# Kernel optimization log

Hardware: AMD Instinct MI355X
Metric: run time of the kernel (lower is better)

## Reference

```python
import jax, jax.numpy as jnp
import numpy as np

D_MODEL, N_HEADS, HEAD_DIM, D_STATE, CHUNK, N_GROUPS = 3584, 112, 64, 64, 256, 2


def setup_inputs() -> dict:
    key = jax.random.key(0)
    ks = jax.random.split(key, 8)
    b, l = 1, 4096
    inner = N_HEADS * HEAD_DIM
    scale = 0.02  # keep activations well-scaled (nn.Linear-ish init)
    return {
        "hidden_states": jax.random.normal(ks[0], (b, l, D_MODEL), jnp.float32),
        "W_in": jax.random.normal(ks[1], (2 * inner, D_MODEL), jnp.float32) * scale,
        "W_out": jax.random.normal(ks[2], (D_MODEL, inner), jnp.float32) * scale,
        "A_log": jax.random.normal(ks[3], (N_HEADS,), jnp.float32),
        "D": jnp.ones((N_HEADS,), jnp.float32),
        "dt_bias": jax.random.normal(ks[4], (N_HEADS,), jnp.float32),
        "B": jax.random.normal(ks[5], (b, l, N_GROUPS, D_STATE), jnp.float32),
        "C": jax.random.normal(ks[6], (b, l, N_GROUPS, D_STATE), jnp.float32),
    }


def _segsum(x):
    # x: [..., T] -> [..., T, T]; segsum[i,j] = sum_{j<k<=i} x[k], -inf above diag
    T = x.shape[-1]
    cs = jnp.cumsum(x, axis=-1)
    diff = cs[..., :, None] - cs[..., None, :]
    mask = jnp.tril(jnp.ones((T, T), bool))
    return jnp.where(mask, diff, -jnp.inf)


def reference(hidden_states, W_in, W_out, A_log, D, dt_bias, B, C):
    b, l, _ = hidden_states.shape
    h, p, n, c = N_HEADS, HEAD_DIM, D_STATE, CHUNK
    nc = l // c

    xz = hidden_states @ W_in.T                       # [b,l,2*h*p]
    x, z = jnp.split(xz, 2, axis=-1)
    x = x.reshape(b, l, h, p)

    dt = jnp.full((b, l, h), 0.1, hidden_states.dtype)  # module uses constant 0.1
    A = -jnp.exp(A_log)                                  # [h]
    dt_sp = jax.nn.softplus(dt + dt_bias)                # [b,l,h]

    # expand group-shared B/C to per-head
    Bh = jnp.repeat(B, h // N_GROUPS, axis=2)            # [b,l,h,n]
    Ch = jnp.repeat(C, h // N_GROUPS, axis=2)

    xdt = x * dt_sp[..., None]                           # discretized input dt*x

    # chunked views: k = chunk index, i/j = position within chunk
    xc = xdt.reshape(b, nc, c, h, p)
    Bc = Bh.reshape(b, nc, c, h, n)
    Cc = Ch.reshape(b, nc, c, h, n)
    dA = (dt_sp * A).reshape(b, nc, c, h).transpose(0, 3, 1, 2)  # [b,h,nc,c]
    dA_cs = jnp.cumsum(dA, axis=-1)                               # [b,h,nc,c]

    # 1) intra-chunk (diagonal blocks)
    L = jnp.exp(_segsum(dA))                                      # [b,h,nc,c,c]
    Y_diag = jnp.einsum('bkihn,bkjhn,bhkij,bkjhp->bkihp', Cc, Bc, L, xc)

    # 2) per-chunk end states
    decay_states = jnp.exp(dA_cs[..., -1:] - dA_cs)               # [b,h,nc,c]
    states = jnp.einsum('bkjhn,bhkj,bkjhp->bkhpn', Bc, decay_states, xc)

    # 3) inter-chunk recurrence: S_k = exp(sum dA_k) * S_{k-1} + states_k
    chunk_decay = jnp.exp(dA_cs[..., -1])                         # [b,h,nc]

    def step(carry, inp):
        dec, st = inp                      # dec: [b,h], st: [b,h,p,n]
        new = carry * dec[..., None, None] + st
        return new, carry                  # emit state ENTERING this chunk

    _, prev = jax.lax.scan(
        step,
        jnp.zeros_like(states[:, 0]),
        (chunk_decay.transpose(2, 0, 1), states.transpose(1, 0, 2, 3, 4)),
    )
    prev = prev.transpose(1, 0, 2, 3, 4)                          # [b,nc,h,p,n]

    # 4) inter-chunk output contribution
    Y_off = jnp.einsum('bkihn,bkhpn,bhki->bkihp', Cc, prev, jnp.exp(dA_cs))

    y = (Y_diag + Y_off).reshape(b, l, h, p) + x * D[None, None, :, None]
    y = y.reshape(b, l, h * p) * jax.nn.sigmoid(z)                # gated
    return y @ W_out.T
```

## Files before the change

### kernel.cpp

```cpp
#include <hip/hip_runtime.h>
#include <hip/hip_bf16.h>

typedef __bf16 bf16;
typedef bf16 bf16x4 __attribute__((ext_vector_type(4)));
typedef bf16 bf16x8 __attribute__((ext_vector_type(8)));
typedef float f32x4 __attribute__((ext_vector_type(4)));

#define GLDS(g, l)                                                            \
  __builtin_amdgcn_global_load_lds(                                           \
      (const __attribute__((address_space(1))) void*)(g),                     \
      (__attribute__((address_space(3))) void*)(l), 16, 0, 0)

constexpr int DM = 3584;
constexpr int NH = 112;
constexpr int HD = 64;
constexpr int DSTATE = 64;
constexpr int CH = 256;
constexpr int NG = 2;
constexpr int SEQ = 4096;
constexpr int INNER = NH * HD;
constexpr int NCHUNK = SEQ / CH;
constexpr int HPG = NH / NG;

__device__ __forceinline__ float softplus_f(float x) {
  return x > 15.f ? x : log1pf(expf(x));
}

__device__ __forceinline__ f32x4 mfma_bf16(bf16x8 a, bf16x8 b, f32x4 c) {
  return __builtin_amdgcn_mfma_f32_16x16x32_bf16(a, b, c, 0, 0, 0);
}

__device__ __forceinline__ void wgbar() {
  asm volatile("" ::: "memory");
  __builtin_amdgcn_s_barrier();
  asm volatile("" ::: "memory");
}

__global__ __launch_bounds__(256) void k_cvt(const float* __restrict__ in,
                                             bf16* __restrict__ out, int n4) {
  int i = blockIdx.x * 256 + threadIdx.x;
  if (i >= n4) return;
  float4 v = reinterpret_cast<const float4*>(in)[i];
  bf16x4 o;
  o[0] = (bf16)v.x; o[1] = (bf16)v.y; o[2] = (bf16)v.z; o[3] = (bf16)v.w;
  reinterpret_cast<bf16x4*>(out)[i] = o;
}

template <int MODE>
__global__ __launch_bounds__(512, 2) void k_gemm(const bf16* __restrict__ A,
                                                 const bf16* __restrict__ B,
                                                 void* __restrict__ outp, int K) {
  __shared__ alignas(16) bf16 lds[65536];
  char* ldsb = (char*)lds;

  const int t = threadIdx.x;
  const int lane = t & 63, wv = t >> 6;
  const int wm = wv >> 2, wn = wv & 3;
  const int l16 = lane & 15, quad = lane >> 4;

  const int gx = gridDim.x, gy = gridDim.y;
  const int orig = blockIdx.y * gx + blockIdx.x;
  long m0, n0;
  if ((gx % 2) == 0 && (gy % 4) == 0) {
    const int xcd = orig & 7;
    const int l = orig >> 3;
    const int xc = xcd & 1, xr = xcd >> 1;
    const int RN = gx >> 1, RM = gy >> 2;
    const int lm = l & (RM - 1);
    const int ln = l >> 2;
    m0 = (long)(xr * RM + lm) * 256;
    n0 = (long)(xc * RN + ln) * 256;
  } else {
    n0 = (long)blockIdx.x * 256;
    m0 = (long)blockIdx.y * 256;
  }

  const int r2 = t >> 3;
  const int cgl = (t & 7) ^ (r2 & 7);
  const int gsr = r2 * 2 + (cgl >> 2);
  const int cel = (cgl & 3) * 8;
  const bf16* pA0 = A + (m0 + gsr) * (size_t)K + cel;
  const bf16* pA1 = pA0 + (size_t)128 * K;
  const bf16* pB0 = B + (n0 + gsr) * (size_t)K + cel;
  const bf16* pB1 = pB0 + (size_t)128 * K;

  const int swzr = (((l16 & 1) << 2) + quad) ^ ((l16 >> 1) & 7);
  const int offA = (wm * 64 + (l16 >> 1)) * 128 + swzr * 16;
  const int offB = (wn * 32 + (l16 >> 1)) * 128 + swzr * 16;

  f32x4 acc[8][4] = {};
  bf16x8 af[4], bfr[4];
  const int NT = K >> 6;

#define STG_A(koff, slot)                        \
  GLDS(pA0 + (koff), ldsb + (slot) + t * 16);    \
  GLDS(pA1 + (koff), ldsb + (slot) + 8192 + t * 16)
#define STG_B(koff, slot)                        \
  GLDS(pB0 + (koff), ldsb + (slot) + t * 16);    \
  GLDS(pB1 + (koff), ldsb + (slot) + 8192 + t * 16)
#define LD_A(mh, slot)                                                 \
  _Pragma("unroll") for (int mf = 0; mf < 4; ++mf)                     \
      af[mf] = *reinterpret_cast<const bf16x8*>(                       \
          ldsb + (slot) + offA + ((mh) * 4 + mf) * 1024)
#define LD_B(slot)                                                     \
  _Pragma("unroll") for (int nf = 0; nf < 4; ++nf)                     \
      bfr[nf] = *reinterpret_cast<const bf16x8*>(                      \
          ldsb + (slot) + offB + nf * 1024)
#define MFMA16(mh)                                                     \
  __builtin_amdgcn_s_setprio(1);                                       \
  _Pragma("unroll") for (int mf = 0; mf < 4; ++mf)                     \
      _Pragma("unroll") for (int nf = 0; nf < 4; ++nf)                 \
          acc[(mh) * 4 + mf][nf] =                                     \
              mfma_bf16(af[mf], bfr[nf], acc[(mh) * 4 + mf][nf]);      \
  __builtin_amdgcn_s_setprio(0)
#define VMW(n) asm volatile("s_waitcnt vmcnt(" #n ")" ::: "memory")

  STG_A(0, 0);
  STG_B(0, 65536);
  STG_A(32, 16384);
  STG_B(32, 65536 + 16384);
  STG_A(64, 32768);
  STG_B(64, 65536 + 32768);
  VMW(8);
  wgbar();

  int buf = 0;
  for (int tt = 0; tt < NT; ++tt, buf ^= 1) {
    const int aB = buf * 32768, oB = 32768 - aB;
    const int sA0 = aB, sA1 = aB + 16384;
    const int sB0 = 65536 + aB, sB1 = 65536 + aB + 16384;
    const int oA1 = oB + 16384, oB1 = 65536 + oB + 16384;
    const int k1 = (tt + 1) * 64 + 32;
    const int k2 = (tt + 2) * 64;

    if (tt + 1 < NT) { STG_A(k1, oA1); }
    LD_B(sB0);
    LD_A(0, sA0);
    wgbar();
    MFMA16(0);
    wgbar();
    if (tt + 1 < NT) { STG_B(k1, oB1); }
    LD_A(1, sA0);
    wgbar();
    MFMA16(1);
    if (tt + 1 < NT) { VMW(8); } else { VMW(0); }
    wgbar();
    if (tt + 2 < NT) { STG_A(k2, sA0); }
    LD_B(sB1);
    LD_A(0, sA1);
    wgbar();
    MFMA16(0);
    wgbar();
    if (tt + 2 < NT) { STG_B(k2, sB0); }
    LD_A(1, sA1);
    wgbar();
    MFMA16(1);
    if (tt + 2 < NT) { VMW(8); }
    else if (tt + 1 < NT) { VMW(4); }
    wgbar();
  }

#undef STG_A
#undef STG_B
#undef LD_A
#undef LD_B
#undef MFMA16
#undef VMW

#pragma unroll
  for (int mf = 0; mf < 8; ++mf)
#pragma unroll
    for (int nf = 0; nf < 4; ++nf) {
      long col = n0 + wn * 64 + nf * 16 + l16;
      long mg = m0 + wm * 128 + mf * 16 + quad * 4;
      if constexpr (MODE == 0) {
        bf16* o = (bf16*)outp;
        bf16x4 v;
#pragma unroll
        for (int u = 0; u < 4; u++) v[u] = (bf16)acc[mf][nf][u];
        *reinterpret_cast<bf16x4*>(&o[col * SEQ + mg]) = v;
      } else if constexpr (MODE == 1) {
        bf16* o = (bf16*)outp;
#pragma unroll
        for (int u = 0; u < 4; u++)
          o[(mg + u) * (long)INNER + col] = (bf16)acc[mf][nf][u];
      } else {
        float* o = (float*)outp;
#pragma unroll
        for (int u = 0; u < 4; u++)
          o[(mg + u) * (long)DM + col] = acc[mf][nf][u];
      }
    }
}

__global__ __launch_bounds__(256) void k_states(const bf16* __restrict__ xT,
                                                const bf16* __restrict__ Bbf,
                                                const float* __restrict__ A_log,
                                                const float* __restrict__ dt_bias,
                                                float* __restrict__ states) {
  const int kc = blockIdx.x;
  const int h = blockIdx.y;
  const int g = h / HPG;
  const int t = threadIdx.x;
  const int wave = t >> 6, lane = t & 63, quad = lane >> 4, l16 = lane & 15;
  const float dts = softplus_f(0.1f + dt_bias[h]);
  const float dAh = -expf(A_log[h]) * dts;

  __shared__ alignas(16) bf16 xTs[64 * 136];
  __shared__ alignas(16) bf16 BTs[64 * 136];

  const bf16* srcX = xT + (size_t)h * 64 * SEQ + (size_t)kc * CH;
  const bf16* srcB = Bbf + ((size_t)kc * CH * NG + g) * DSTATE;

  f32x4 acc[4] = {};

  for (int half = 0; half < 2; half++) {
    __syncthreads();
#pragma unroll
    for (int q = 0; q < 4; q++) {
      int u = q * 256 + t;
      int row = u >> 4, c8 = (u & 15) * 8;
      bf16x8 v = *reinterpret_cast<const bf16x8*>(&srcX[(size_t)row * SEQ + half * 128 + c8]);
      *reinterpret_cast<bf16x8*>(&xTs[row * 136 + c8]) = v;
    }
#pragma unroll
    for (int q = 0; q < 4; q++) {
      int u = q * 256 + t;
      int jl = u & 127, n8 = (u >> 7) * 8;
      int j = half * 128 + jl;
      bf16x8 v = *reinterpret_cast<const bf16x8*>(&srcB[(size_t)j * (NG * DSTATE) + n8]);
      float s = expf(dAh * (float)(CH - 1 - j));
#pragma unroll
      for (int e = 0; e < 8; e++)
        BTs[(n8 + e) * 136 + jl] = (bf16)((float)v[e] * s);
    }
    __syncthreads();
#pragma unroll
    for (int kk = 0; kk < 4; kk++) {
      bf16x8 a = *reinterpret_cast<const bf16x8*>(&xTs[(wave * 16 + l16) * 136 + kk * 32 + quad * 8]);
#pragma unroll
      for (int tn = 0; tn < 4; tn++) {
        bf16x8 b = *reinterpret_cast<const bf16x8*>(&BTs[(tn * 16 + l16) * 136 + kk * 32 + quad * 8]);
        acc[tn] = mfma_bf16(a, b, acc[tn]);
      }
    }
  }
  float* dst = states + (size_t)(kc * NH + h) * 64 * 64;
#pragma unroll
  for (int tn = 0; tn < 4; tn++)
#pragma unroll
    for (int u = 0; u < 4; u++) {
      int p = wave * 16 + quad * 4 + u;
      dst[p * 64 + tn * 16 + l16] = acc[tn][u] * dts;
    }
}

__global__ __launch_bounds__(256) void k_scan(float* __restrict__ states,
                                              const float* __restrict__ A_log,
                                              const float* __restrict__ dt_bias) {
  int idx = blockIdx.x * 256 + threadIdx.x;
  int h = idx >> 12;
  int pn = idx & 4095;
  float dts = softplus_f(0.1f + dt_bias[h]);
  float dAh = -expf(A_log[h]) * dts;
  float cd = expf(dAh * (float)CH);
  float carry = 0.f;
  float* p = states + (size_t)h * 4096 + pn;
  const size_t stride = (size_t)NH * 4096;
#pragma unroll
  for (int k = 0; k < NCHUNK; k++) {
    float s = p[k * stride];
    p[k * stride] = carry;
    carry = carry * cd + s;
  }
}

__global__ __launch_bounds__(256) void k_y(const bf16* __restrict__ xT,
                                           const bf16* __restrict__ Bbf,
                                           const bf16* __restrict__ Cbf,
                                           const float* __restrict__ prev,
                                           bf16* __restrict__ zy,
                                           const float* __restrict__ A_log,
                                           const float* __restrict__ Dvec,
                                           const float* __restrict__ dt_bias) {
  const int half = blockIdx.x;
  const int kc = blockIdx.y;
  const int h = blockIdx.z;
  const int g = h / HPG;
  const int i0 = half * 128;
  const int t = threadIdx.x;
  const int wave = t >> 6, lane = t & 63, quad = lane >> 4, l16 = lane & 15;
  const float dts = softplus_f(0.1f + dt_bias[h]);
  const float dAh = -expf(A_log[h]) * dts;
  const float Dh = Dvec[h];

  __shared__ alignas(16) bf16 Cs[128 * 72];
  __shared__ alignas(16) bf16 Bsh[64 * 72];
  __shared__ alignas(16) bf16 xTs[64 * 72];
  __shared__ alignas(16) bf16 Ws[128 * 72];

  {
    const bf16* src = Cbf + ((size_t)(kc * CH + i0) * NG + g) * DSTATE;
#pragma unroll
    for (int q = 0; q < 4; q++) {
      int u = q * 256 + t;
      int row = u >> 3, c8 = (u & 7) * 8;
      bf16x8 v = *reinterpret_cast<const bf16x8*>(&src[(size_t)row * (NG * DSTATE) + c8]);
      *reinterpret_cast<bf16x8*>(&Cs[row * 72 + c8]) = v;
    }
  }
  {
    const float* src = prev + (size_t)(kc * NH + h) * 4096;
#pragma unroll
    for (int q = 0; q < 4; q++) {
      int u = q * 256 + t;
      int p = u >> 4, c4 = (u & 15) * 4;
      float4 v = *reinterpret_cast<const float4*>(&src[p * 64 + c4]);
      bf16x4 o;
      o[0] = (bf16)v.x; o[1] = (bf16)v.y; o[2] = (bf16)v.z; o[3] = (bf16)v.w;
      *reinterpret_cast<bf16x4*>(&Bsh[p * 72 + c4]) = o;
    }
  }
  __syncthreads();

  f32x4 accY[2][4] = {};
#pragma unroll
  for (int kk = 0; kk < 2; kk++) {
    bf16x8 a0 = *reinterpret_cast<const bf16x8*>(&Cs[(wave * 32 + l16) * 72 + kk * 32 + quad * 8]);
    bf16x8 a1 = *reinterpret_cast<const bf16x8*>(&Cs[(wave * 32 + 16 + l16) * 72 + kk * 32 + quad * 8]);
#pragma unroll
    for (int tn = 0; tn < 4; tn++) {
      bf16x8 b = *reinterpret_cast<const bf16x8*>(&Bsh[(tn * 16 + l16) * 72 + kk * 32 + quad * 8]);
      accY[0][tn] = mfma_bf16(a0, b, accY[0][tn]);
      accY[1][tn] = mfma_bf16(a1, b, accY[1][tn]);
    }
  }
#pragma unroll
  for (int tm = 0; tm < 2; tm++)
#pragma unroll
    for (int u = 0; u < 4; u++) {
      float sc = expf(dAh * (float)(i0 + wave * 32 + tm * 16 + quad * 4 + u + 1));
#pragma unroll
      for (int tn = 0; tn < 4; tn++) accY[tm][tn][u] *= sc;
    }

  const int npan = half ? 4 : 2;
  for (int jb = 0; jb < npan; jb++) {
    __syncthreads();
    {
      const bf16* src = Bbf + ((size_t)(kc * CH + jb * 64) * NG + g) * DSTATE;
#pragma unroll
      for (int q = 0; q < 2; q++) {
        int u = q * 256 + t;
        int row = u >> 3, c8 = (u & 7) * 8;
        bf16x8 v = *reinterpret_cast<const bf16x8*>(&src[(size_t)row * (NG * DSTATE) + c8]);
        *reinterpret_cast<bf16x8*>(&Bsh[row * 72 + c8]) = v;
      }
    }
    {
      const bf16* src = xT + (size_t)h * 64 * SEQ + (size_t)kc * CH + jb * 64;
#pragma unroll
      for (int q = 0; q < 2; q++) {
        int u = q * 256 + t;
        int row = u >> 3, c8 = (u & 7) * 8;
        bf16x8 v = *reinterpret_cast<const bf16x8*>(&src[(size_t)row * SEQ + c8]);
        *reinterpret_cast<bf16x8*>(&xTs[row * 72 + c8]) = v;
      }
    }
    __syncthreads();
    f32x4 accS[2][4] = {};
#pragma unroll
    for (int kk = 0; kk < 2; kk++) {
      bf16x8 a0 = *reinterpret_cast<const bf16x8*>(&Cs[(wave * 32 + l16) * 72 + kk * 32 + quad * 8]);
      bf16x8 a1 = *reinterpret_cast<const bf16x8*>(&Cs[(wave * 32 + 16 + l16) * 72 + kk * 32 + quad * 8]);
#pragma unroll
      for (int tj = 0; tj < 4; tj++) {
        bf16x8 b = *reinterpret_cast<const bf16x8*>(&Bsh[(tj * 16 + l16) * 72 + kk * 32 + quad * 8]);
        accS[0][tj] = mfma_bf16(a0, b, accS[0][tj]);
        accS[1][tj] = mfma_bf16(a1, b, accS[1][tj]);
      }
    }
#pragma unroll
    for (int tm = 0; tm < 2; tm++)
#pragma unroll
      for (int tj = 0; tj < 4; tj++)
#pragma unroll
        for (int u = 0; u < 4; u++) {
          int li = wave * 32 + tm * 16 + quad * 4 + u;
          int ai = i0 + li;
          int aj = jb * 64 + tj * 16 + l16;
          float s = (ai >= aj) ? dts * expf(dAh * (float)(ai - aj)) : 0.f;
          Ws[li * 72 + tj * 16 + l16] = (bf16)(accS[tm][tj][u] * s);
        }
#pragma unroll
    for (int kk = 0; kk < 2; kk++) {
      bf16x8 a0 = *reinterpret_cast<const bf16x8*>(&Ws[(wave * 32 + l16) * 72 + kk * 32 + quad * 8]);
      bf16x8 a1 = *reinterpret_cast<const bf16x8*>(&Ws[(wave * 32 + 16 + l16) * 72 + kk * 32 + quad * 8]);
#pragma unroll
      for (int tn = 0; tn < 4; tn++) {
        bf16x8 b = *reinterpret_cast<const bf16x8*>(&xTs[(tn * 16 + l16) * 72 + kk * 32 + quad * 8]);
        accY[0][tn] = mfma_bf16(a0, b, accY[0][tn]);
        accY[1][tn] = mfma_bf16(a1, b, accY[1][tn]);
      }
    }
  }

#pragma unroll
  for (int tm = 0; tm < 2; tm++)
#pragma unroll
    for (int tn = 0; tn < 4; tn++)
#pragma unroll
      for (int u = 0; u < 4; u++) {
        int li = wave * 32 + tm * 16 + quad * 4 + u;
        long lg = (long)kc * CH + i0 + li;
        int p = tn * 16 + l16;
        float xv = (float)xT[(size_t)(h * 64 + p) * SEQ + lg];
        float yv = accY[tm][tn][u] + xv * Dh;
        size_t off = (size_t)lg * INNER + h * 64 + p;
        float zv = (float)zy[off];
        float gate = 1.f / (1.f + expf(-zv));
        zy[off] = (bf16)(yv * gate);
      }
}

extern "C" void kernel_launch(void* const* d_in, const int* in_sizes, int n_in,
                              void* d_out, int out_size, void* d_ws, size_t ws_size,
                              hipStream_t stream) {
  const float* hs    = (const float*)d_in[0];
  const float* W_in  = (const float*)d_in[1];
  const float* W_out = (const float*)d_in[2];
  const float* A_log = (const float*)d_in[3];
  const float* Dv    = (const float*)d_in[4];
  const float* dtb   = (const float*)d_in[5];
  const float* Bin   = (const float*)d_in[6];
  const float* Cin   = (const float*)d_in[7];

  char* ws = (char*)d_ws;
  size_t off = 0;
  auto alloc = [&](size_t bytes) {
    void* p = ws + off;
    off += (bytes + 255) & ~(size_t)255;
    return p;
  };
  bf16* wbuf = (bf16*)alloc((size_t)INNER * DM * 2);
  bf16* hsb  = (bf16*)alloc((size_t)SEQ * DM * 2);
  bf16* xTg  = (bf16*)alloc((size_t)INNER * SEQ * 2);
  bf16* zy   = (bf16*)alloc((size_t)SEQ * INNER * 2);
  bf16* Bbf  = (bf16*)alloc((size_t)SEQ * NG * DSTATE * 2);
  bf16* Cbf  = (bf16*)alloc((size_t)SEQ * NG * DSTATE * 2);
  float* st  = (float*)alloc((size_t)NCHUNK * NH * 64 * 64 * 4);

  auto cvt = [&](const float* src, bf16* dst, size_t n) {
    int n4 = (int)(n / 4);
    k_cvt<<<dim3((n4 + 255) / 256), dim3(256), 0, stream>>>(src, dst, n4);
  };

  cvt(hs, hsb, (size_t)SEQ * DM);
  cvt(Bin, Bbf, (size_t)SEQ * NG * DSTATE);
  cvt(Cin, Cbf, (size_t)SEQ * NG * DSTATE);

  dim3 blk(256);
  dim3 gblk(512);
  dim3 g1(INNER / 256, SEQ / 256);
  dim3 g2(DM / 256, SEQ / 256);

  cvt(W_in, wbuf, (size_t)INNER * DM);
  k_gemm<0><<<g1, gblk, 0, stream>>>(hsb, wbuf, xTg, DM);
  cvt(W_in + (size_t)INNER * DM, wbuf, (size_t)INNER * DM);
  k_gemm<1><<<g1, gblk, 0, stream>>>(hsb, wbuf, zy, DM);
  cvt(W_out, wbuf, (size_t)DM * INNER);

  k_states<<<dim3(NCHUNK, NH), blk, 0, stream>>>(xTg, Bbf, A_log, dtb, st);
  k_scan<<<dim3((NH * 4096) / 256), blk, 0, stream>>>(st, A_log, dtb);
  k_y<<<dim3(2, NCHUNK, NH), blk, 0, stream>>>(xTg, Bbf, Cbf, st, zy, A_log, Dv, dtb);

  k_gemm<2><<<g2, gblk, 0, stream>>>(zy, wbuf, d_out, INNER);

  (void)in_sizes; (void)n_in; (void)out_size; (void)ws_size;
}
```

Measured before the change: 1.162 ms.

## Double-buffer GEMM register fragments to overlap LDS reads with MFMA

The A and B fragment registers in the bf16 GEMM main loop become two register sets. LDS reads for the next MFMA block are issued before the current block's MFMAs, and the first fragments are prefetched before the loop. The goal is to hide LDS read latency behind matrix-core work instead of stalling on each read/compute barrier pair. In exchange it uses more VGPRs, which may lower occupancy, and it reorders barriers and vmcnt waits in a way that could introduce LDS hazards if misordered.

```diff
diff --git a/kernel.cpp b/kernel.cpp
--- a/kernel.cpp
+++ b/kernel.cpp
@@ -89,7 +89,7 @@
   const int offB = (wn * 32 + (l16 >> 1)) * 128 + swzr * 16;
 
   f32x4 acc[8][4] = {};
-  bf16x8 af[4], bfr[4];
+  bf16x8 af[2][4], bfr[2][4];
   const int NT = K >> 6;
 
 #define STG_A(koff, slot)                        \
@@ -98,20 +98,20 @@
 #define STG_B(koff, slot)                        \
   GLDS(pB0 + (koff), ldsb + (slot) + t * 16);    \
   GLDS(pB1 + (koff), ldsb + (slot) + 8192 + t * 16)
-#define LD_A(mh, slot)                                                 \
+#define LD_A(set, mh, slot)                                            \
   _Pragma("unroll") for (int mf = 0; mf < 4; ++mf)                     \
-      af[mf] = *reinterpret_cast<const bf16x8*>(                       \
+      af[set][mf] = *reinterpret_cast<const bf16x8*>(                  \
           ldsb + (slot) + offA + ((mh) * 4 + mf) * 1024)
-#define LD_B(slot)                                                     \
+#define LD_B(set, slot)                                                \
   _Pragma("unroll") for (int nf = 0; nf < 4; ++nf)                     \
-      bfr[nf] = *reinterpret_cast<const bf16x8*>(                      \
+      bfr[set][nf] = *reinterpret_cast<const bf16x8*>(                 \
           ldsb + (slot) + offB + nf * 1024)
-#define MFMA16(mh)                                                     \
+#define MFMA16(mh, as_, bs_)                                           \
   __builtin_amdgcn_s_setprio(1);                                       \
   _Pragma("unroll") for (int mf = 0; mf < 4; ++mf)                     \
       _Pragma("unroll") for (int nf = 0; nf < 4; ++nf)                 \
-          acc[(mh) * 4 + mf][nf] =                                     \
-              mfma_bf16(af[mf], bfr[nf], acc[(mh) * 4 + mf][nf]);      \
+          acc[(mh) * 4 + mf][nf] = mfma_bf16(af[as_][mf], bfr[bs_][nf],\
+                                             acc[(mh) * 4 + mf][nf]);  \
   __builtin_amdgcn_s_setprio(0)
 #define VMW(n) asm volatile("s_waitcnt vmcnt(" #n ")" ::: "memory")
 
@@ -123,40 +123,43 @@
   STG_B(64, 65536 + 32768);
   VMW(8);
   wgbar();
+  LD_B(0, 65536);
+  LD_A(0, 0, 0);
 
   int buf = 0;
   for (int tt = 0; tt < NT; ++tt, buf ^= 1) {
     const int aB = buf * 32768, oB = 32768 - aB;
     const int sA0 = aB, sA1 = aB + 16384;
     const int sB0 = 65536 + aB, sB1 = 65536 + aB + 16384;
-    const int oA1 = oB + 16384, oB1 = 65536 + oB + 16384;
+    const int oA0 = oB, oA1 = oB + 16384;
+    const int oB0 = 65536 + oB, oB1 = 65536 + oB + 16384;
     const int k1 = (tt + 1) * 64 + 32;
     const int k2 = (tt + 2) * 64;
 
     if (tt + 1 < NT) { STG_A(k1, oA1); }
-    LD_B(sB0);
-    LD_A(0, sA0);
-    wgbar();
-    MFMA16(0);
-    wgbar();
-    if (tt + 1 < NT) { STG_B(k1, oB1); }
-    LD_A(1, sA0);
-    wgbar();
-    MFMA16(1);
-    if (tt + 1 < NT) { VMW(8); } else { VMW(0); }
+    wgbar();
+    LD_A(1, 1, sA0);
+    MFMA16(0, 0, 0);
+    wgbar();
+    if (tt + 1 < NT) { STG_B(k1, oB1); VMW(8); } else { VMW(0); }
+    wgbar();
+    LD_B(1, sB1);
+    LD_A(0, 0, sA1);
+    MFMA16(1, 1, 0);
     wgbar();
     if (tt + 2 < NT) { STG_A(k2, sA0); }
-    LD_B(sB1);
-    LD_A(0, sA1);
-    wgbar();
-    MFMA16(0);
-    wgbar();
-    if (tt + 2 < NT) { STG_B(k2, sB0); }
-    LD_A(1, sA1);
-    wgbar();
-    MFMA16(1);
-    if (tt + 2 < NT) { VMW(8); }
+    wgbar();
+    LD_A(1, 1, sA1);
+    MFMA16(0, 0, 1);
+    wgbar();
+    if (tt + 2 < NT) { STG_B(k2, sB0); VMW(8); }
     else if (tt + 1 < NT) { VMW(4); }
+    wgbar();
+    if (tt + 1 < NT) {
+      LD_B(0, oB0);
+      LD_A(0, 0, oA0);
+    }
+    MFMA16(1, 1, 1);
     wgbar();
   }
 
```

Measured after the change: 1.184 ms. No clear change (+1.9%).
